# Kernel optimization log

Hardware: AMD Instinct MI355X
Metric: run time of the kernel (lower is better)

The kernel has to match this reference:

```python
import jax, jax.numpy as jnp
import numpy as np

D = 1024

def setup_inputs() -> dict:
    key = jax.random.key(0)
    ks = jax.random.split(key, 7)
    s = 1.0 / np.sqrt(D)  # torch Linear default init scale (uniform bound)
    x = jax.random.normal(ks[0], (4, 2048, D), dtype=jnp.float32)
    Wq = jax.random.uniform(ks[1], (D, D), jnp.float32, -s, s)
    Wk = jax.random.uniform(ks[2], (D, D), jnp.float32, -s, s)
    Wv = jax.random.uniform(ks[3], (D, D), jnp.float32, -s, s)
    bq = jax.random.uniform(ks[4], (D,), jnp.float32, -s, s)
    bk = jax.random.uniform(ks[5], (D,), jnp.float32, -s, s)
    bv = jax.random.uniform(ks[6], (D,), jnp.float32, -s, s)
    return {"x": x, "Wq": Wq, "bq": bq, "Wk": Wk, "bk": bk, "Wv": Wv, "bv": bv}

def reference(x, Wq, bq, Wk, bk, Wv, bv):
    # Linear layers: y = x @ W^T + b (weights stored torch-style [out, in])
    Q = jnp.einsum('bsd,ed->bse', x, Wq) + bq
    K = jnp.einsum('bsd,ed->bse', x, Wk) + bk
    V = jnp.einsum('bsd,ed->bse', x, Wv) + bv
    scale = jnp.sqrt(jnp.asarray(Q.shape[-1], Q.dtype))
    scores = jnp.einsum('bqd,bkd->bqk', Q, K) / scale  # [B, S, S]
    probs = jax.nn.softmax(scores, axis=-1)
    return jnp.einsum('bqk,bkd->bqd', probs, V)
```

## Files before the change

### kernel.cpp

```cpp
#include <hip/hip_runtime.h>


typedef __bf16 bf16x8 __attribute__((ext_vector_type(8)));
typedef float f32x4 __attribute__((ext_vector_type(4)));
typedef unsigned short u16;

__device__ __forceinline__ u16 f2b(float f) {
  union { float f; unsigned u; } a; a.f = f;
  unsigned r = a.u + 0x7fffu + ((a.u >> 16) & 1u);
  return (u16)(r >> 16);
}

__global__ __launch_bounds__(256) void cast_all_kernel(const float* __restrict__ x,
                                                       const float* __restrict__ Wq,
                                                       const float* __restrict__ Wk,
                                                       const float* __restrict__ Wv,
                                                       u16* __restrict__ xb,
                                                       u16* __restrict__ Wb) {
  int b = blockIdx.x;
  if (b < 8192) {
    const int i = b * 256 + threadIdx.x;
    float4 v = reinterpret_cast<const float4*>(x)[i];
    reinterpret_cast<ushort4*>(xb)[i] =
        make_ushort4(f2b(v.x), f2b(v.y), f2b(v.z), f2b(v.w));
  } else {
    b -= 8192;
    const int w = b >> 10;
    const float* src = (w == 0) ? Wq : (w == 1) ? Wk : Wv;
    const int i = (b & 1023) * 256 + threadIdx.x;
    float4 v = reinterpret_cast<const float4*>(src)[i];
    reinterpret_cast<ushort4*>(Wb + (size_t)w * 1048576)[i] =
        make_ushort4(f2b(v.x), f2b(v.y), f2b(v.z), f2b(v.w));
  }
}

template <int GEOM, int NT>
__device__ __forceinline__ void core2(const char* __restrict__ Ab,
                                      const char* __restrict__ Bb, int lda, int ldb,
                                      char* smem, f32x4* acc) {
  constexpr int LDSBUF = GEOM ? 49152 : 65536;
  constexpr int BOFF = GEOM ? 16384 : 32768;
  constexpr int AHALF = GEOM ? 8192 : 16384;
  constexpr int NA = GEOM ? 4 : 8;
  const int tid = threadIdx.x;
  const int wave = tid >> 6, lane = tid & 63;
  const int wr = wave >> 2, wc = wave & 3;
  const int fr = lane & 15, fg = lane >> 4;
  const int rd = (fr * 64 + fg * 16) ^ (((fr >> 3) & 1) << 5);
  const int li = (lane * 16) ^ ((lane >> 5) << 5);
  const int sr = li >> 6, sc2 = li & 63;

  auto STAGE = [&](int kt, int s) {
    char* base = smem + (kt & 1) * LDSBUF;
    const int colOff = kt * 128 + s * 64 + sc2;
    char* ldsA = base + s * AHALF;
    __builtin_amdgcn_global_load_lds(
        (const __attribute__((address_space(1))) void*)(Ab + (size_t)(wave * 16 + sr) * lda + colOff),
        (__attribute__((address_space(3))) void*)(ldsA + wave * 1024), 16, 0, 0);
    if constexpr (GEOM == 0)
      __builtin_amdgcn_global_load_lds(
          (const __attribute__((address_space(1))) void*)(Ab + (size_t)((8 + wave) * 16 + sr) * lda + colOff),
          (__attribute__((address_space(3))) void*)(ldsA + 8192 + wave * 1024), 16, 0, 0);
    char* ldsB = base + BOFF + s * 16384;
    __builtin_amdgcn_global_load_lds(
        (const __attribute__((address_space(1))) void*)(Bb + (size_t)(wave * 16 + sr) * ldb + colOff),
        (__attribute__((address_space(3))) void*)(ldsB + wave * 1024), 16, 0, 0);
    __builtin_amdgcn_global_load_lds(
        (const __attribute__((address_space(1))) void*)(Bb + (size_t)((8 + wave) * 16 + sr) * ldb + colOff),
        (__attribute__((address_space(3))) void*)(ldsB + 8192 + wave * 1024), 16, 0, 0);
  };

  STAGE(0, 0);
  STAGE(0, 1);
  if constexpr (GEOM == 0) asm volatile("s_waitcnt vmcnt(4)" ::: "memory");
  else asm volatile("s_waitcnt vmcnt(3)" ::: "memory");
  __builtin_amdgcn_s_barrier();
  __builtin_amdgcn_sched_barrier(0);

  for (int kt = 0; kt < NT; ++kt) {
    const char* bufA = smem + (kt & 1) * LDSBUF;
    const char* bufB = bufA + BOFF;
#pragma unroll
    for (int s = 0; s < 2; ++s) {
      bf16x8 afr[NA], bfr[4];
#pragma unroll
      for (int m = 0; m < NA; ++m)
        afr[m] = *reinterpret_cast<const bf16x8*>(bufA + s * AHALF + (wr * NA + m) * 1024 + rd);
#pragma unroll
      for (int n = 0; n < 4; ++n)
        bfr[n] = *reinterpret_cast<const bf16x8*>(bufB + s * 16384 + (wc * 4 + n) * 1024 + rd);
      if (kt + 1 < NT) STAGE(kt + 1, s);
      __builtin_amdgcn_s_barrier();
      __builtin_amdgcn_sched_barrier(0);
      __builtin_amdgcn_s_setprio(1);
#pragma unroll
      for (int m = 0; m < NA; ++m)
#pragma unroll
        for (int n = 0; n < 4; ++n)
          acc[m * 4 + n] = __builtin_amdgcn_mfma_f32_16x16x32_bf16(
              afr[m], bfr[n], acc[m * 4 + n], 0, 0, 0);
      __builtin_amdgcn_s_setprio(0);
      if (kt < NT - 1) {
        if constexpr (GEOM == 0) asm volatile("s_waitcnt vmcnt(4)" ::: "memory");
        else asm volatile("s_waitcnt vmcnt(3)" ::: "memory");
      } else if (s == 0) {
        asm volatile("s_waitcnt vmcnt(0)" ::: "memory");
      }
      __builtin_amdgcn_s_barrier();
      __builtin_amdgcn_sched_barrier(0);
    }
  }
}

__global__ __launch_bounds__(512, 2) void qkproj_kernel(
    const u16* __restrict__ A, const u16* __restrict__ Bm,
    const float* __restrict__ bq, const float* __restrict__ bk,
    u16* __restrict__ QK) {
  extern __shared__ char smem[];
  const int tileM = blockIdx.x * 256, tileN = blockIdx.y * 256;
  f32x4 acc[32] = {};
  core2<0, 16>((const char*)A + (size_t)tileM * 2048,
               (const char*)Bm + (size_t)tileN * 2048, 2048, 2048, smem, acc);
  const int tid = threadIdx.x;
  const int wave = tid >> 6, lane = tid & 63;
  const int wr = wave >> 2, wc = wave & 3, fr = lane & 15, fg = lane >> 4;
  const int w = blockIdx.y >> 2;
  const float* bias = (w == 0) ? bq : bk;
  u16* O = QK + (size_t)w * 8388608;
#pragma unroll
  for (int mi = 0; mi < 8; ++mi) {
    const int r0 = tileM + wr * 128 + mi * 16 + fg * 4;
#pragma unroll
    for (int n = 0; n < 4; ++n) {
      const int cw = (tileN + wc * 64 + n * 16 + fr) & 1023;
      const float bi = bias[cw];
#pragma unroll
      for (int jj = 0; jj < 4; ++jj)
        O[(size_t)(r0 + jj) * 1024 + cw] = f2b(acc[mi * 4 + n][jj] + bi);
    }
  }
}

__global__ __launch_bounds__(512, 2) void vproj_kernel(
    const u16* __restrict__ A, const u16* __restrict__ Bv,
    const float* __restrict__ bvv, u16* __restrict__ Vt) {
  extern __shared__ char smem[];
  const int tileM = blockIdx.x * 128, tileN = blockIdx.y * 256;
  f32x4 acc[16] = {};
  core2<1, 16>((const char*)A + (size_t)tileM * 2048,
               (const char*)Bv + (size_t)tileN * 2048, 2048, 2048, smem, acc);
  const int tid = threadIdx.x;
  const int wave = tid >> 6, lane = tid & 63;
  const int wr = wave >> 2, wc = wave & 3, fr = lane & 15, fg = lane >> 4;
#pragma unroll
  for (int mi = 0; mi < 4; ++mi) {
    const int r0 = tileM + wr * 64 + mi * 16 + fg * 4;
    const int b = r0 >> 11, s0 = r0 & 2047;
#pragma unroll
    for (int n = 0; n < 4; ++n) {
      const int cw = (tileN + wc * 64 + n * 16 + fr) & 1023;
      const float bi = bvv[cw];
      ushort4 u = make_ushort4(f2b(acc[mi * 4 + n][0] + bi), f2b(acc[mi * 4 + n][1] + bi),
                               f2b(acc[mi * 4 + n][2] + bi), f2b(acc[mi * 4 + n][3] + bi));
      *reinterpret_cast<ushort4*>(&Vt[(size_t)b * 2097152 + (size_t)cw * 2048 + s0]) = u;
    }
  }
}

__global__ __launch_bounds__(512, 2) void sc8_kernel(const u16* __restrict__ Qb,
                                                     const u16* __restrict__ Kb,
                                                     u16* __restrict__ P,
                                                     float* __restrict__ rowpart) {
  extern __shared__ char smem[];
  const int z = blockIdx.z;
  const int tileM = blockIdx.x * 256, tileN = blockIdx.y * 256;
  f32x4 acc[32] = {};
  core2<0, 16>((const char*)Qb + (size_t)z * 4194304 + (size_t)tileM * 2048,
               (const char*)Kb + (size_t)z * 4194304 + (size_t)tileN * 2048, 2048, 2048,
               smem, acc);
  const int tid = threadIdx.x;
  const int wave = tid >> 6, lane = tid & 63;
  const int wr = wave >> 2, wc = wave & 3, fr = lane & 15, fg = lane >> 4;
  float* rs = (float*)smem;
  u16* Po = P + (size_t)z * 4194304 + (size_t)tileM * 2048 + tileN;
#pragma unroll
  for (int mi = 0; mi < 8; ++mi) {
#pragma unroll
    for (int jj = 0; jj < 4; ++jj) {
      const int rl = wr * 128 + mi * 16 + fg * 4 + jj;
      float part = 0.f;
#pragma unroll
      for (int n = 0; n < 4; ++n) {
        float e = __expf(acc[mi * 4 + n][jj] * 0.03125f);
        part += e;
        Po[(size_t)rl * 2048 + wc * 64 + n * 16 + fr] = f2b(e);
      }
      part += __shfl_xor(part, 1);
      part += __shfl_xor(part, 2);
      part += __shfl_xor(part, 4);
      part += __shfl_xor(part, 8);
      if (fr == 0) rs[wc * 256 + rl] = part;
    }
  }
  __syncthreads();
  if (tid < 256) {
    float s = rs[tid] + rs[256 + tid] + rs[512 + tid] + rs[768 + tid];
    rowpart[(size_t)blockIdx.y * 8192 + z * 2048 + tileM + tid] = s;
  }
}

__global__ __launch_bounds__(512, 2) void pv8_kernel(const u16* __restrict__ P,
                                                     const u16* __restrict__ Vt,
                                                     const float* __restrict__ rowpart,
                                                     float* __restrict__ out) {
  extern __shared__ char smem[];
  const int z = blockIdx.z;
  const int tileM = blockIdx.x * 128, tileN = blockIdx.y * 256;
  float* rinv = (float*)(smem + 98304);
  const int tid = threadIdx.x;
  if (tid < 128) {
    float s = 0.f;
#pragma unroll
    for (int t = 0; t < 8; ++t) s += rowpart[t * 8192 + z * 2048 + tileM + tid];
    rinv[tid] = 1.0f / s;
  }
  __builtin_amdgcn_sched_barrier(0);
  f32x4 acc[16] = {};
  core2<1, 32>((const char*)P + (size_t)z * 8388608 + (size_t)tileM * 4096,
               (const char*)Vt + (size_t)z * 4194304 + (size_t)tileN * 4096, 4096, 4096,
               smem, acc);
  const int wave = tid >> 6, lane = tid & 63;
  const int wr = wave >> 2, wc = wave & 3, fr = lane & 15, fg = lane >> 4;
  float* O = out + (size_t)z * 2097152;
#pragma unroll
  for (int mi = 0; mi < 4; ++mi) {
#pragma unroll
    for (int jj = 0; jj < 4; ++jj) {
      const int r = wr * 64 + mi * 16 + fg * 4 + jj;
      const float inv = rinv[r];
#pragma unroll
      for (int n = 0; n < 4; ++n)
        O[(size_t)(tileM + r) * 1024 + tileN + wc * 64 + n * 16 + fr] =
            acc[mi * 4 + n][jj] * inv;
    }
  }
}

extern "C" void kernel_launch(void* const* d_in, const int* in_sizes, int n_in,
                              void* d_out, int out_size, void* d_ws, size_t ws_size,
                              hipStream_t stream) {
  if (ws_size < ((size_t)72 << 20)) return;
  const float* x = (const float*)d_in[0];
  const float* Wq = (const float*)d_in[1];
  const float* bq = (const float*)d_in[2];
  const float* Wk = (const float*)d_in[3];
  const float* bk = (const float*)d_in[4];
  const float* Wv = (const float*)d_in[5];
  const float* bv = (const float*)d_in[6];
  char* ws = (char*)d_ws;
  u16* xb = (u16*)(ws);
  u16* Pb = (u16*)(ws);
  u16* Qb = (u16*)(ws + ((size_t)16 << 20));
  u16* Kb = (u16*)(ws + ((size_t)32 << 20));
  u16* Vt = (u16*)(ws + ((size_t)48 << 20));
  u16* Wb = (u16*)(ws + ((size_t)64 << 20));
  float* rowpart = (float*)(ws + ((size_t)70 << 20));
  float* out = (float*)d_out;

  (void)hipFuncSetAttribute((const void*)qkproj_kernel,
                            hipFuncAttributeMaxDynamicSharedMemorySize, 131072);
  (void)hipFuncSetAttribute((const void*)vproj_kernel,
                            hipFuncAttributeMaxDynamicSharedMemorySize, 98304);
  (void)hipFuncSetAttribute((const void*)sc8_kernel,
                            hipFuncAttributeMaxDynamicSharedMemorySize, 131072);
  (void)hipFuncSetAttribute((const void*)pv8_kernel,
                            hipFuncAttributeMaxDynamicSharedMemorySize, 98816);

  cast_all_kernel<<<11264, 256, 0, stream>>>(x, Wq, Wk, Wv, xb, Wb);

  qkproj_kernel<<<dim3(32, 8), 512, 131072, stream>>>(xb, Wb, bq, bk, Qb);
  vproj_kernel<<<dim3(64, 4), 512, 98304, stream>>>(xb, Wb + 2097152, bv, Vt);

  sc8_kernel<<<dim3(8, 8, 4), 512, 131072, stream>>>(Qb, Kb, Pb, rowpart);
  pv8_kernel<<<dim3(16, 4, 4), 512, 98816, stream>>>(Pb, Vt, rowpart, out);
}
```

Baseline: 155.9 us.

## Switch GEMM core from 16x16x32 to 32x32x16 bf16 MFMA tiles

Replaces the 16x16x32 MFMA instruction with the 32x32x16 variant across all four GEMM kernels. The LDS fragment reads, accumulator layout and epilogue row/column mapping are reworked to match, and the softmax row-sum reduction gains an extra shuffle. Larger MFMA tiles need fewer LDS fragment loads per FLOP and fewer instructions issued. The cost is a different accumulator layout whose epilogue stores are less contiguous, and the LDS read pattern may hit bank conflicts.

```diff
diff --git a/kernel.cpp b/kernel.cpp
--- a/kernel.cpp
+++ b/kernel.cpp
@@ -2,7 +2,7 @@
 
 
 typedef __bf16 bf16x8 __attribute__((ext_vector_type(8)));
-typedef float f32x4 __attribute__((ext_vector_type(4)));
+typedef float f32x16 __attribute__((ext_vector_type(16)));
 typedef unsigned short u16;
 
 __device__ __forceinline__ u16 f2b(float f) {
@@ -37,16 +37,16 @@
 template <int GEOM, int NT>
 __device__ __forceinline__ void core2(const char* __restrict__ Ab,
                                       const char* __restrict__ Bb, int lda, int ldb,
-                                      char* smem, f32x4* acc) {
+                                      char* smem, f32x16* acc) {
   constexpr int LDSBUF = GEOM ? 49152 : 65536;
   constexpr int BOFF = GEOM ? 16384 : 32768;
   constexpr int AHALF = GEOM ? 8192 : 16384;
-  constexpr int NA = GEOM ? 4 : 8;
+  constexpr int NMI = GEOM ? 2 : 4;
   const int tid = threadIdx.x;
   const int wave = tid >> 6, lane = tid & 63;
   const int wr = wave >> 2, wc = wave & 3;
-  const int fr = lane & 15, fg = lane >> 4;
-  const int rd = (fr * 64 + fg * 16) ^ (((fr >> 3) & 1) << 5);
+  const int hi16 = (lane >> 4) & 1;
+  const int rdbase = (((lane & 15) * 64 + (lane >> 5) * 16)) ^ (((lane >> 3) & 1) << 5);
   const int li = (lane * 16) ^ ((lane >> 5) << 5);
   const int sr = li >> 6, sc2 = li & 63;
 
@@ -82,23 +82,35 @@
     const char* bufB = bufA + BOFF;
 #pragma unroll
     for (int s = 0; s < 2; ++s) {
-      bf16x8 afr[NA], bfr[4];
-#pragma unroll
-      for (int m = 0; m < NA; ++m)
-        afr[m] = *reinterpret_cast<const bf16x8*>(bufA + s * AHALF + (wr * NA + m) * 1024 + rd);
-#pragma unroll
-      for (int n = 0; n < 4; ++n)
-        bfr[n] = *reinterpret_cast<const bf16x8*>(bufB + s * 16384 + (wc * 4 + n) * 1024 + rd);
+      bf16x8 afr[2 * NMI], bfr[4];
+#pragma unroll
+      for (int ks = 0; ks < 2; ++ks) {
+        const int inner = rdbase ^ (ks << 5);
+#pragma unroll
+        for (int mi = 0; mi < NMI; ++mi) {
+          const int sub = wr * (GEOM ? 4 : 8) + mi * 2 + hi16;
+          afr[ks * NMI + mi] =
+              *reinterpret_cast<const bf16x8*>(bufA + s * AHALF + sub * 1024 + inner);
+        }
+#pragma unroll
+        for (int ni = 0; ni < 2; ++ni) {
+          const int sub = wc * 4 + ni * 2 + hi16;
+          bfr[ks * 2 + ni] =
+              *reinterpret_cast<const bf16x8*>(bufB + s * 16384 + sub * 1024 + inner);
+        }
+      }
       if (kt + 1 < NT) STAGE(kt + 1, s);
       __builtin_amdgcn_s_barrier();
       __builtin_amdgcn_sched_barrier(0);
       __builtin_amdgcn_s_setprio(1);
 #pragma unroll
-      for (int m = 0; m < NA; ++m)
-#pragma unroll
-        for (int n = 0; n < 4; ++n)
-          acc[m * 4 + n] = __builtin_amdgcn_mfma_f32_16x16x32_bf16(
-              afr[m], bfr[n], acc[m * 4 + n], 0, 0, 0);
+      for (int ks = 0; ks < 2; ++ks)
+#pragma unroll
+        for (int mi = 0; mi < NMI; ++mi)
+#pragma unroll
+          for (int ni = 0; ni < 2; ++ni)
+            acc[mi * 2 + ni] = __builtin_amdgcn_mfma_f32_32x32x16_bf16(
+                afr[ks * NMI + mi], bfr[ks * 2 + ni], acc[mi * 2 + ni], 0, 0, 0);
       __builtin_amdgcn_s_setprio(0);
       if (kt < NT - 1) {
         if constexpr (GEOM == 0) asm volatile("s_waitcnt vmcnt(4)" ::: "memory");
@@ -112,31 +124,34 @@
   }
 }
 
+#define CROW(reg, hi) (((reg) & 3) + 8 * ((reg) >> 2) + 4 * (hi))
+
 __global__ __launch_bounds__(512, 2) void qkproj_kernel(
     const u16* __restrict__ A, const u16* __restrict__ Bm,
     const float* __restrict__ bq, const float* __restrict__ bk,
     u16* __restrict__ QK) {
   extern __shared__ char smem[];
   const int tileM = blockIdx.x * 256, tileN = blockIdx.y * 256;
-  f32x4 acc[32] = {};
+  f32x16 acc[8] = {};
   core2<0, 16>((const char*)A + (size_t)tileM * 2048,
                (const char*)Bm + (size_t)tileN * 2048, 2048, 2048, smem, acc);
   const int tid = threadIdx.x;
   const int wave = tid >> 6, lane = tid & 63;
-  const int wr = wave >> 2, wc = wave & 3, fr = lane & 15, fg = lane >> 4;
+  const int wr = wave >> 2, wc = wave & 3, hi = lane >> 5, c31 = lane & 31;
   const int w = blockIdx.y >> 2;
   const float* bias = (w == 0) ? bq : bk;
   u16* O = QK + (size_t)w * 8388608;
 #pragma unroll
-  for (int mi = 0; mi < 8; ++mi) {
-    const int r0 = tileM + wr * 128 + mi * 16 + fg * 4;
-#pragma unroll
-    for (int n = 0; n < 4; ++n) {
-      const int cw = (tileN + wc * 64 + n * 16 + fr) & 1023;
+  for (int mi = 0; mi < 4; ++mi) {
+#pragma unroll
+    for (int ni = 0; ni < 2; ++ni) {
+      const int cw = (tileN + wc * 64 + ni * 32 + c31) & 1023;
       const float bi = bias[cw];
 #pragma unroll
-      for (int jj = 0; jj < 4; ++jj)
-        O[(size_t)(r0 + jj) * 1024 + cw] = f2b(acc[mi * 4 + n][jj] + bi);
+      for (int reg = 0; reg < 16; ++reg) {
+        const int row = tileM + wr * 128 + mi * 32 + CROW(reg, hi);
+        O[(size_t)row * 1024 + cw] = f2b(acc[mi * 2 + ni][reg] + bi);
+      }
     }
   }
 }
@@ -146,23 +161,27 @@
     const float* __restrict__ bvv, u16* __restrict__ Vt) {
   extern __shared__ char smem[];
   const int tileM = blockIdx.x * 128, tileN = blockIdx.y * 256;
-  f32x4 acc[16] = {};
+  f32x16 acc[4] = {};
   core2<1, 16>((const char*)A + (size_t)tileM * 2048,
                (const char*)Bv + (size_t)tileN * 2048, 2048, 2048, smem, acc);
   const int tid = threadIdx.x;
   const int wave = tid >> 6, lane = tid & 63;
-  const int wr = wave >> 2, wc = wave & 3, fr = lane & 15, fg = lane >> 4;
-#pragma unroll
-  for (int mi = 0; mi < 4; ++mi) {
-    const int r0 = tileM + wr * 64 + mi * 16 + fg * 4;
-    const int b = r0 >> 11, s0 = r0 & 2047;
-#pragma unroll
-    for (int n = 0; n < 4; ++n) {
-      const int cw = (tileN + wc * 64 + n * 16 + fr) & 1023;
+  const int wr = wave >> 2, wc = wave & 3, hi = lane >> 5, c31 = lane & 31;
+#pragma unroll
+  for (int mi = 0; mi < 2; ++mi) {
+#pragma unroll
+    for (int ni = 0; ni < 2; ++ni) {
+      const int cw = (tileN + wc * 64 + ni * 32 + c31) & 1023;
       const float bi = bvv[cw];
-      ushort4 u = make_ushort4(f2b(acc[mi * 4 + n][0] + bi), f2b(acc[mi * 4 + n][1] + bi),
-                               f2b(acc[mi * 4 + n][2] + bi), f2b(acc[mi * 4 + n][3] + bi));
-      *reinterpret_cast<ushort4*>(&Vt[(size_t)b * 2097152 + (size_t)cw * 2048 + s0]) = u;
+#pragma unroll
+      for (int q = 0; q < 4; ++q) {
+        const int r0 = tileM + wr * 64 + mi * 32 + 8 * q + 4 * hi;
+        const int b = r0 >> 11, s0 = r0 & 2047;
+        ushort4 u = make_ushort4(
+            f2b(acc[mi * 2 + ni][q * 4 + 0] + bi), f2b(acc[mi * 2 + ni][q * 4 + 1] + bi),
+            f2b(acc[mi * 2 + ni][q * 4 + 2] + bi), f2b(acc[mi * 2 + ni][q * 4 + 3] + bi));
+        *reinterpret_cast<ushort4*>(&Vt[(size_t)b * 2097152 + (size_t)cw * 2048 + s0]) = u;
+      }
     }
   }
 }
@@ -174,32 +193,31 @@
   extern __shared__ char smem[];
   const int z = blockIdx.z;
   const int tileM = blockIdx.x * 256, tileN = blockIdx.y * 256;
-  f32x4 acc[32] = {};
+  f32x16 acc[8] = {};
   core2<0, 16>((const char*)Qb + (size_t)z * 4194304 + (size_t)tileM * 2048,
                (const char*)Kb + (size_t)z * 4194304 + (size_t)tileN * 2048, 2048, 2048,
                smem, acc);
   const int tid = threadIdx.x;
   const int wave = tid >> 6, lane = tid & 63;
-  const int wr = wave >> 2, wc = wave & 3, fr = lane & 15, fg = lane >> 4;
+  const int wr = wave >> 2, wc = wave & 3, hi = lane >> 5, c31 = lane & 31;
   float* rs = (float*)smem;
   u16* Po = P + (size_t)z * 4194304 + (size_t)tileM * 2048 + tileN;
 #pragma unroll
-  for (int mi = 0; mi < 8; ++mi) {
-#pragma unroll
-    for (int jj = 0; jj < 4; ++jj) {
-      const int rl = wr * 128 + mi * 16 + fg * 4 + jj;
-      float part = 0.f;
-#pragma unroll
-      for (int n = 0; n < 4; ++n) {
-        float e = __expf(acc[mi * 4 + n][jj] * 0.03125f);
-        part += e;
-        Po[(size_t)rl * 2048 + wc * 64 + n * 16 + fr] = f2b(e);
-      }
+  for (int mi = 0; mi < 4; ++mi) {
+#pragma unroll
+    for (int reg = 0; reg < 16; ++reg) {
+      const int rl = wr * 128 + mi * 32 + CROW(reg, hi);
+      const float e0 = __expf(acc[mi * 2 + 0][reg] * 0.03125f);
+      const float e1 = __expf(acc[mi * 2 + 1][reg] * 0.03125f);
+      Po[(size_t)rl * 2048 + wc * 64 + c31] = f2b(e0);
+      Po[(size_t)rl * 2048 + wc * 64 + 32 + c31] = f2b(e1);
+      float part = e0 + e1;
       part += __shfl_xor(part, 1);
       part += __shfl_xor(part, 2);
       part += __shfl_xor(part, 4);
       part += __shfl_xor(part, 8);
-      if (fr == 0) rs[wc * 256 + rl] = part;
+      part += __shfl_xor(part, 16);
+      if (c31 == 0) rs[wc * 256 + rl] = part;
     }
   }
   __syncthreads();
@@ -225,23 +243,23 @@
     rinv[tid] = 1.0f / s;
   }
   __builtin_amdgcn_sched_barrier(0);
-  f32x4 acc[16] = {};
+  f32x16 acc[4] = {};
   core2<1, 32>((const char*)P + (size_t)z * 8388608 + (size_t)tileM * 4096,
                (const char*)Vt + (size_t)z * 4194304 + (size_t)tileN * 4096, 4096, 4096,
                smem, acc);
   const int wave = tid >> 6, lane = tid & 63;
-  const int wr = wave >> 2, wc = wave & 3, fr = lane & 15, fg = lane >> 4;
+  const int wr = wave >> 2, wc = wave & 3, hi = lane >> 5, c31 = lane & 31;
   float* O = out + (size_t)z * 2097152;
 #pragma unroll
-  for (int mi = 0; mi < 4; ++mi) {
-#pragma unroll
-    for (int jj = 0; jj < 4; ++jj) {
-      const int r = wr * 64 + mi * 16 + fg * 4 + jj;
-      const float inv = rinv[r];
-#pragma unroll
-      for (int n = 0; n < 4; ++n)
-        O[(size_t)(tileM + r) * 1024 + tileN + wc * 64 + n * 16 + fr] =
-            acc[mi * 4 + n][jj] * inv;
+  for (int mi = 0; mi < 2; ++mi) {
+#pragma unroll
+    for (int ni = 0; ni < 2; ++ni) {
+#pragma unroll
+      for (int reg = 0; reg < 16; ++reg) {
+        const int r = wr * 64 + mi * 32 + CROW(reg, hi);
+        O[(size_t)(tileM + r) * 1024 + tileN + wc * 64 + ni * 32 + c31] =
+            acc[mi * 2 + ni][reg] * rinv[r];
+      }
     }
   }
 }
```

After: 173.7 us. 1.11x slower.
